# Optimization experiments

Measured on AMD Instinct MI355X. Metric: run time of the kernel, lower is better.

The kernel has to match this reference:

```python
import jax, jax.numpy as jnp
import numpy as np

HIDDEN = 512
H2 = HIDDEN * 2  # 1024
SEQ = 65536


def setup_inputs() -> dict:
    key = jax.random.key(0)
    k0, k1, k2, k3 = jax.random.split(key, 4)
    outputs = jax.random.normal(k0, (SEQ, H2), dtype=jnp.float32)
    # nn.Linear(2H, 2H): weight [out, in], bias [out]
    lim = 1.0 / np.sqrt(H2)
    W = jax.random.uniform(k1, (H2, H2), dtype=jnp.float32, minval=-lim, maxval=lim)
    b = jax.random.uniform(k2, (H2,), dtype=jnp.float32, minval=-lim, maxval=lim)
    weight_vec = jax.random.normal(k3, (1, H2), dtype=jnp.float32)
    return {"outputs": outputs, "W": W, "b": b, "weight_vec": weight_vec}


def reference(outputs, W, b, weight_vec):
    # energy_i = dot(weight_vec, W @ outputs[i] + b)  -> batched:
    energy = jnp.einsum("sh,oh->so", outputs, W) + b          # [S, 2H]
    attn_energies = energy @ weight_vec.reshape(-1)            # [S]
    attn = jax.nn.softmax(attn_energies, axis=0)               # [S]
    return attn[None, None, :]                                 # [1, 1, S]
```

## Files before the change

### kernel.cpp

```cpp
#include <hip/hip_runtime.h>
#include <hip/hip_bf16.h>
#include <math.h>

#define SEQ   65536
#define H2    1024
#define OCHUNKS 64
#define OPER   (H2 / OCHUNKS)

__global__ void reduce_W_partial(const float* __restrict__ W,
                                 const float* __restrict__ wv,
                                 float* __restrict__ partial) {
    int h = blockIdx.x * 256 + threadIdx.x;
    int oc = blockIdx.y;
    int o0 = oc * OPER;
    float acc = 0.0f;
#pragma unroll
    for (int j = 0; j < OPER; ++j) {
        int o = o0 + j;
        acc += wv[o] * W[(size_t)o * H2 + h];
    }
    partial[(size_t)oc * H2 + h] = acc;
}

__global__ void reduce_partial_to_v(const float* __restrict__ partial,
                                    float* __restrict__ v) {
    int h = blockIdx.x * 256 + threadIdx.x;
    float acc = 0.0f;
#pragma unroll 8
    for (int oc = 0; oc < OCHUNKS; ++oc)
        acc += partial[(size_t)oc * H2 + h];
    v[h] = acc;
}

__global__ void row_dot(const float4* __restrict__ outputs,
                        const float4* __restrict__ v4,
                        float* __restrict__ e) {
    int gtid = blockIdx.x * blockDim.x + threadIdx.x;
    int row  = gtid >> 6;
    int lane = threadIdx.x & 63;

    const float4* rp = outputs + (size_t)row * (H2 / 4);
    float acc = 0.0f;
#pragma unroll
    for (int i = 0; i < 4; ++i) {
        float4 a = rp[lane + 64 * i];
        float4 b = v4[lane + 64 * i];
        acc += a.x * b.x + a.y * b.y + a.z * b.z + a.w * b.w;
    }
#pragma unroll
    for (int off = 32; off > 0; off >>= 1)
        acc += __shfl_down(acc, off, 64);
    if (lane == 0) e[row] = acc;
}

__global__ void softmax_stats(const float* __restrict__ e,
                              float* __restrict__ stats) {
    __shared__ float red[16];
    __shared__ float gmax_sh;
    int tid  = threadIdx.x;
    int wid  = tid >> 6;
    int lane = tid & 63;

    float m = -INFINITY;
    for (int i = tid; i < SEQ; i += 1024) m = fmaxf(m, e[i]);
#pragma unroll
    for (int off = 32; off > 0; off >>= 1)
        m = fmaxf(m, __shfl_down(m, off, 64));
    if (lane == 0) red[wid] = m;
    __syncthreads();
    if (tid == 0) {
        float mm = red[0];
#pragma unroll
        for (int w = 1; w < 16; ++w) mm = fmaxf(mm, red[w]);
        gmax_sh = mm;
    }
    __syncthreads();
    float gmax = gmax_sh;

    float s = 0.0f;
    for (int i = tid; i < SEQ; i += 1024) s += __expf(e[i] - gmax);
#pragma unroll
    for (int off = 32; off > 0; off >>= 1)
        s += __shfl_down(s, off, 64);
    if (lane == 0) red[wid] = s;
    __syncthreads();
    if (tid == 0) {
        float ss = 0.0f;
#pragma unroll
        for (int w = 0; w < 16; ++w) ss += red[w];
        stats[0] = gmax;
        stats[1] = 1.0f / ss;
    }
}

__global__ void softmax_norm(const float* __restrict__ e,
                             const float* __restrict__ stats,
                             float* __restrict__ out) {
    int i = blockIdx.x * blockDim.x + threadIdx.x;
    float gmax = stats[0];
    float inv  = stats[1];
    out[i] = __expf(e[i] - gmax) * inv;
}

extern "C" void kernel_launch(void* const* d_in, const int* in_sizes, int n_in,
                              void* d_out, int out_size, void* d_ws, size_t ws_size,
                              hipStream_t stream) {
    const float* outputs = (const float*)d_in[0];
    const float* W       = (const float*)d_in[1];
    const float* wv      = (const float*)d_in[3];
    float* out = (float*)d_out;

    float* ws = (float*)d_ws;
    float* v       = ws;
    float* partial = ws + H2;
    float* e       = ws + H2 + OCHUNKS * H2;
    float* stats   = e + SEQ;

    reduce_W_partial<<<dim3(4, OCHUNKS), 256, 0, stream>>>(W, wv, partial);
    reduce_partial_to_v<<<4, 256, 0, stream>>>(partial, v);
    row_dot<<<SEQ / 4, 256, 0, stream>>>((const float4*)outputs,
                                         (const float4*)v, e);
    softmax_stats<<<1, 1024, 0, stream>>>(e, stats);
    softmax_norm<<<SEQ / 256, 256, 0, stream>>>(e, stats, out);
}
```

Measured before the change: 383.3 us.

## Fuse online softmax max/sum into row_dot and shrink stats kernel

The row_dot kernel now processes 16 rows per wavefront with v kept in registers. It computes per-block online-softmax max and sum alongside the energies, and writes those partials to workspace. softmax_stats then only merges 1024 block partials instead of scanning all 65536 energies twice in a single block, which removes a serial bottleneck. The trade-off is fewer blocks in row_dot (1024) and extra exp work per row.

```diff
diff --git a/kernel.cpp b/kernel.cpp
--- a/kernel.cpp
+++ b/kernel.cpp
@@ -1,105 +1,124 @@
 #include <hip/hip_runtime.h>
-#include <hip/hip_bf16.h>
 #include <math.h>
 
-#define SEQ   65536
-#define H2    1024
-#define OCHUNKS 64
-#define OPER   (H2 / OCHUNKS)
+#define SEQ 65536
+#define H2  1024
 
 __global__ void reduce_W_partial(const float* __restrict__ W,
                                  const float* __restrict__ wv,
                                  float* __restrict__ partial) {
-    int h = blockIdx.x * 256 + threadIdx.x;
-    int oc = blockIdx.y;
-    int o0 = oc * OPER;
+    const int h  = blockIdx.x * 256 + threadIdx.x;
+    const int oc = blockIdx.y;
+    const int o0 = oc * 16;
     float acc = 0.0f;
 #pragma unroll
-    for (int j = 0; j < OPER; ++j) {
-        int o = o0 + j;
-        acc += wv[o] * W[(size_t)o * H2 + h];
-    }
-    partial[(size_t)oc * H2 + h] = acc;
+    for (int j = 0; j < 16; ++j)
+        acc += wv[o0 + j] * W[(size_t)(o0 + j) * H2 + h];
+    partial[oc * H2 + h] = acc;
 }
 
-__global__ void reduce_partial_to_v(const float* __restrict__ partial,
-                                    float* __restrict__ v) {
-    int h = blockIdx.x * 256 + threadIdx.x;
+__global__ void fold_v(const float* __restrict__ partial,
+                       float* __restrict__ v) {
+    const int h = blockIdx.x * 256 + threadIdx.x;
     float acc = 0.0f;
 #pragma unroll 8
-    for (int oc = 0; oc < OCHUNKS; ++oc)
-        acc += partial[(size_t)oc * H2 + h];
+    for (int oc = 0; oc < 64; ++oc) acc += partial[oc * H2 + h];
     v[h] = acc;
 }
 
-__global__ void row_dot(const float4* __restrict__ outputs,
-                        const float4* __restrict__ v4,
-                        float* __restrict__ e) {
-    int gtid = blockIdx.x * blockDim.x + threadIdx.x;
-    int row  = gtid >> 6;
-    int lane = threadIdx.x & 63;
+__global__ void __launch_bounds__(256) row_dot(
+        const float4* __restrict__ outputs,
+        const float4* __restrict__ v4,
+        float* __restrict__ e,
+        float* __restrict__ bmax,
+        float* __restrict__ bsum) {
+    const int b    = blockIdx.x;
+    const int t    = threadIdx.x;
+    const int w    = t >> 6;
+    const int lane = t & 63;
 
-    const float4* rp = outputs + (size_t)row * (H2 / 4);
-    float acc = 0.0f;
+    const float4 vr0 = v4[lane];
+    const float4 vr1 = v4[lane + 64];
+    const float4 vr2 = v4[lane + 128];
+    const float4 vr3 = v4[lane + 192];
+
+    const int r0 = b * 64 + w * 16;
+    float m = -INFINITY, s = 0.0f, myval = 0.0f;
+
+#pragma unroll 4
+    for (int j = 0; j < 16; ++j) {
+        const float4* rp = outputs + (size_t)(r0 + j) * 256;
+        const float4 a0 = rp[lane];
+        const float4 a1 = rp[lane + 64];
+        const float4 a2 = rp[lane + 128];
+        const float4 a3 = rp[lane + 192];
+        float acc = a0.x * vr0.x + a0.y * vr0.y + a0.z * vr0.z + a0.w * vr0.w;
+        acc      += a1.x * vr1.x + a1.y * vr1.y + a1.z * vr1.z + a1.w * vr1.w;
+        acc      += a2.x * vr2.x + a2.y * vr2.y + a2.z * vr2.z + a2.w * vr2.w;
+        acc      += a3.x * vr3.x + a3.y * vr3.y + a3.z * vr3.z + a3.w * vr3.w;
+#pragma unroll
+        for (int off = 1; off < 64; off <<= 1)
+            acc += __shfl_xor(acc, off, 64);
+        if (lane == j) myval = acc;
+        const float d = acc - m;
+        if (d > 0.0f) { s = s * __expf(-d) + 1.0f; m = acc; }
+        else          { s += __expf(d); }
+    }
+    if (lane < 16) e[r0 + lane] = myval;
+
+    __shared__ float lm[4], ls[4];
+    if (lane == 0) { lm[w] = m; ls[w] = s; }
+    __syncthreads();
+    if (t == 0) {
+        float M = lm[0], S = ls[0];
+#pragma unroll
+        for (int i = 1; i < 4; ++i) {
+            const float Mn = fmaxf(M, lm[i]);
+            S = S * __expf(M - Mn) + ls[i] * __expf(lm[i] - Mn);
+            M = Mn;
+        }
+        bmax[b] = M;
+        bsum[b] = S;
+    }
+}
+
+__global__ void softmax_stats(const float* __restrict__ bmax,
+                              const float* __restrict__ bsum,
+                              float* __restrict__ stats) {
+    const int t = threadIdx.x;
+    float M = -INFINITY, S = 0.0f;
 #pragma unroll
     for (int i = 0; i < 4; ++i) {
-        float4 a = rp[lane + 64 * i];
-        float4 b = v4[lane + 64 * i];
-        acc += a.x * b.x + a.y * b.y + a.z * b.z + a.w * b.w;
+        const int idx = t + 256 * i;
+        const float m2 = bmax[idx], s2 = bsum[idx];
+        const float Mn = fmaxf(M, m2);
+        S = S * __expf(M - Mn) + s2 * __expf(m2 - Mn);
+        M = Mn;
     }
-#pragma unroll
-    for (int off = 32; off > 0; off >>= 1)
-        acc += __shfl_down(acc, off, 64);
-    if (lane == 0) e[row] = acc;
-}
-
-__global__ void softmax_stats(const float* __restrict__ e,
-                              float* __restrict__ stats) {
-    __shared__ float red[16];
-    __shared__ float gmax_sh;
-    int tid  = threadIdx.x;
-    int wid  = tid >> 6;
-    int lane = tid & 63;
-
-    float m = -INFINITY;
-    for (int i = tid; i < SEQ; i += 1024) m = fmaxf(m, e[i]);
-#pragma unroll
-    for (int off = 32; off > 0; off >>= 1)
-        m = fmaxf(m, __shfl_down(m, off, 64));
-    if (lane == 0) red[wid] = m;
+    __shared__ float rm[256], rs[256];
+    rm[t] = M; rs[t] = S;
     __syncthreads();
-    if (tid == 0) {
-        float mm = red[0];
-#pragma unroll
-        for (int w = 1; w < 16; ++w) mm = fmaxf(mm, red[w]);
-        gmax_sh = mm;
+    for (int stride = 128; stride > 0; stride >>= 1) {
+        if (t < stride) {
+            const float M1 = rm[t], S1 = rs[t];
+            const float M2 = rm[t + stride], S2 = rs[t + stride];
+            const float Mn = fmaxf(M1, M2);
+            rm[t] = Mn;
+            rs[t] = S1 * __expf(M1 - Mn) + S2 * __expf(M2 - Mn);
+        }
+        __syncthreads();
     }
-    __syncthreads();
-    float gmax = gmax_sh;
-
-    float s = 0.0f;
-    for (int i = tid; i < SEQ; i += 1024) s += __expf(e[i] - gmax);
-#pragma unroll
-    for (int off = 32; off > 0; off >>= 1)
-        s += __shfl_down(s, off, 64);
-    if (lane == 0) red[wid] = s;
-    __syncthreads();
-    if (tid == 0) {
-        float ss = 0.0f;
-#pragma unroll
-        for (int w = 0; w < 16; ++w) ss += red[w];
-        stats[0] = gmax;
-        stats[1] = 1.0f / ss;
+    if (t == 0) {
+        stats[0] = rm[0];
+        stats[1] = 1.0f / rs[0];
     }
 }
 
 __global__ void softmax_norm(const float* __restrict__ e,
                              const float* __restrict__ stats,
                              float* __restrict__ out) {
-    int i = blockIdx.x * blockDim.x + threadIdx.x;
-    float gmax = stats[0];
-    float inv  = stats[1];
-    out[i] = __expf(e[i] - gmax) * inv;
+    const int i = blockIdx.x * 256 + threadIdx.x;
+    out[i] = __expf(e[i] - stats[0]) * stats[1];
 }
 
 extern "C" void kernel_launch(void* const* d_in, const int* in_sizes, int n_in,
@@ -113,13 +132,15 @@
     float* ws = (float*)d_ws;
     float* v       = ws;
     float* partial = ws + H2;
-    float* e       = ws + H2 + OCHUNKS * H2;
-    float* stats   = e + SEQ;
+    float* e       = partial + 64 * H2;
+    float* bmax    = e + SEQ;
+    float* bsum    = bmax + 1024;
+    float* stats   = bsum + 1024;
 
-    reduce_W_partial<<<dim3(4, OCHUNKS), 256, 0, stream>>>(W, wv, partial);
-    reduce_partial_to_v<<<4, 256, 0, stream>>>(partial, v);
-    row_dot<<<SEQ / 4, 256, 0, stream>>>((const float4*)outputs,
-                                         (const float4*)v, e);
-    softmax_stats<<<1, 1024, 0, stream>>>(e, stats);
+    reduce_W_partial<<<dim3(4, 64), 256, 0, stream>>>(W, wv, partial);
+    fold_v<<<4, 256, 0, stream>>>(partial, v);
+    row_dot<<<1024, 256, 0, stream>>>((const float4*)outputs,
+                                      (const float4*)v, e, bmax, bsum);
+    softmax_stats<<<1, 256, 0, stream>>>(bmax, bsum, stats);
     softmax_norm<<<SEQ / 256, 256, 0, stream>>>(e, stats, out);
 }
```

Result: no change. 377.7 us (-1.5%).
